# Optimization experiments

Measured on AMD Instinct MI355X. Metric: run time of the kernel, lower is better.

Reference implementation:

```python
import jax, jax.numpy as jnp
import numpy as np

N_QUBITS = 12
N_LAYERS = 3
N_CHUNKS = 12
CHUNK = 4
BATCH = 2048


def _u3(theta, phi, lam):
    # PennyLane U3 = [[cos(t/2), -e^{i l} sin(t/2)], [e^{i p} sin(t/2), e^{i(p+l)} cos(t/2)]]
    ct = jnp.cos(theta / 2).astype(jnp.complex64)
    st = jnp.sin(theta / 2).astype(jnp.complex64)
    ep = jnp.exp(1j * phi.astype(jnp.complex64))
    el = jnp.exp(1j * lam.astype(jnp.complex64))
    return jnp.stack([jnp.stack([ct, -el * st]), jnp.stack([ep * st, ep * el * ct])])


def _apply_1q(state, U, w):
    # state: (2,)*N_QUBITS
    s = jnp.moveaxis(state, w, 0)
    s = jnp.tensordot(U, s, axes=1)
    return jnp.moveaxis(s, 0, w)


def _apply_cnot(state, c, t):
    s = jnp.moveaxis(state, (c, t), (0, 1))
    s = jnp.stack([s[0], jnp.flip(s[1], axis=0)], axis=0)
    return jnp.moveaxis(s, (0, 1), (c, t))


def _circuit(params):
    # params: [N_CHUNKS, 3] -> expval PauliZ per wire, shape [N_QUBITS]
    state = jnp.zeros((2,) * N_QUBITS, jnp.complex64).at[(0,) * N_QUBITS].set(1.0)
    for _ in range(N_LAYERS):
        for i in range(N_CHUNKS):
            state = _apply_1q(state, _u3(params[i, 0], params[i, 1], params[i, 2]), i)
        for i in range(N_QUBITS):
            state = _apply_cnot(state, i, (i + 1) % N_QUBITS)
    p = jnp.abs(state) ** 2
    sign = jnp.array([1.0, -1.0], p.dtype)
    zs = []
    for i in range(N_QUBITS):
        marg = p.sum(axis=tuple(a for a in range(N_QUBITS) if a != i))
        zs.append(jnp.dot(marg, sign))
    return jnp.stack(zs)


def setup_inputs() -> dict:
    key = jax.random.key(0)
    ks = jax.random.split(key, 7)
    return {
        "x": jax.random.normal(ks[0], (BATCH, 48), jnp.float32),
        "reupload_weights": jax.random.normal(ks[1], (N_CHUNKS, 3, CHUNK), jnp.float32) * 0.1,
        "reupload_bias": jax.random.normal(ks[2], (N_CHUNKS, 3), jnp.float32) * 0.1,
        "w1": jax.random.normal(ks[3], (64, N_QUBITS), jnp.float32) * 0.1,
        "b1": jax.random.normal(ks[4], (64,), jnp.float32) * 0.1,
        "w2": jax.random.normal(ks[5], (256, 64), jnp.float32) * 0.1,
        "b2": jax.random.normal(ks[6], (256,), jnp.float32) * 0.1,
    }


def reference(x, reupload_weights, reupload_bias, w1, b1, w2, b2):
    chunks = x.reshape(-1, N_CHUNKS, CHUNK)  # [B, 12, 4]
    # per-chunk affine map: [12,3,4] @ [B,12,4] -> [B,12,3]
    params = jnp.einsum("cpk,bck->bcp", reupload_weights, chunks) + reupload_bias
    qz = jax.vmap(_circuit)(params)  # [B, 12]
    h = jax.nn.relu(qz @ w1.T + b1)
    return h @ w2.T + b2
```

## Files before the change

kernel.cpp:

```cpp
#include <hip/hip_runtime.h>
#include <hip/hip_fp16.h>
#include <math.h>

typedef _Float16 half8 __attribute__((ext_vector_type(8)));
typedef float f32x4 __attribute__((ext_vector_type(4)));

__device__ __forceinline__ int finv12(int c) {
    return ((c ^ (c << 1)) & 0xFFF) ^ ((c >> 11) * 3);
}
__device__ __forceinline__ int sg0(int s) { return s ^ (((s >> 8) & 1) << 4) ^ (((s >> 9) & 1) << 6); }
__device__ __forceinline__ int sg1(int s) { return s ^ (((s >> 12) & 3) << 4) ^ (((s >> 7) & 1) << 6); }
__device__ __forceinline__ int sg2(int s) { return s ^ (((s >> 8) & 7) << 4); }

__global__ __attribute__((amdgpu_flat_work_group_size(256, 256)))
void qparam_kernel(const float* __restrict__ x, const float* __restrict__ rw,
                   const float* __restrict__ rb, float* __restrict__ uo, int total)
{
    const int g = blockIdx.x * 256 + threadIdx.x;
    if (g >= total) return;
    const int c = g % 12;
    const float4 xv = ((const float4*)x)[g];
    float prm[3];
    #pragma unroll
    for (int p = 0; p < 3; ++p) {
        const float4 wv = ((const float4*)rw)[c * 3 + p];
        prm[p] = rb[c * 3 + p] + wv.x * xv.x + wv.y * xv.y + wv.z * xv.z + wv.w * xv.w;
    }
    float st_, ct_; sincosf(0.5f * prm[0], &st_, &ct_);
    float sp_, cp_; sincosf(prm[1], &sp_, &cp_);
    float sl_, cl_; sincosf(prm[2], &sl_, &cl_);
    const float cpl = cp_ * cl_ - sp_ * sl_;
    const float spl = sp_ * cl_ + cp_ * sl_;
    ((float4*)uo)[g * 2]     = make_float4(ct_, 0.0f, -cl_ * st_, -sl_ * st_);
    ((float4*)uo)[g * 2 + 1] = make_float4(cp_ * st_, sp_ * st_, cpl * ct_, spl * ct_);
}

template<int G>
__device__ __forceinline__ void mfma_pass(
    const char* __restrict__ ldb, char* __restrict__ stb,
    half8 arh, half8 arl, half8 aih, half8 ail,
    int t, int l15, int q, int wv, bool first, bool last,
    float& A0, float& AT0, float& AT01, float& AR0, float& AR01)
{
    #pragma unroll
    for (int T = 0; T < 4; ++T) {
        const int tt = wv * 4 + T;
        half8 bfr;
        if (first) {
            half8 z = {};
            if (t == 0 && T == 0) z[0] = (_Float16)1.0f;
            bfr = z;
        } else {
            int raw4[4];
            #pragma unroll
            for (int j = 0; j < 4; ++j) {
                int byte_;
                if (G == 0) {
                    const int ap = finv12(j | (q << 2) | (l15 << 4) | (tt << 8));
                    byte_ = sg2(64 * (ap & 255) + 4 * ((ap >> 8) & 15));
                } else if (G == 1) {
                    byte_ = sg0(256 * q + 64 * j + 1024 * tt + 4 * l15);
                } else {
                    byte_ = sg1(64 * l15 + 4096 * q + 1024 * j + 4 * tt);
                }
                raw4[j] = *(const int*)(ldb + byte_);
            }
            __builtin_memcpy(&bfr, raw4, 16);
        }
        f32x4 cre = {0.f, 0.f, 0.f, 0.f}, cim = {0.f, 0.f, 0.f, 0.f};
        cre = __builtin_amdgcn_mfma_f32_16x16x32_f16(arh, bfr, cre, 0, 0, 0);
        cre = __builtin_amdgcn_mfma_f32_16x16x32_f16(arl, bfr, cre, 0, 0, 0);
        cim = __builtin_amdgcn_mfma_f32_16x16x32_f16(aih, bfr, cim, 0, 0, 0);
        cim = __builtin_amdgcn_mfma_f32_16x16x32_f16(ail, bfr, cim, 0, 0, 0);
        if (!last) {
            unsigned int ov4[4];
            #pragma unroll
            for (int r = 0; r < 4; ++r) {
                __half2 hp = __floats2half2_rn(cre[r], cim[r]);
                ov4[r] = *(unsigned int*)&hp;
            }
            int4 ov;
            __builtin_memcpy(&ov, ov4, 16);
            const int sb = 1024 * tt + 64 * l15 + 16 * q;
            const int sbyte = (G == 0) ? sg0(sb) : (G == 1) ? sg1(sb) : sg2(sb);
            *(int4*)(stb + sbyte) = ov;
        } else {
            const int sT0 = T & 1, sT01 = (T ^ (T >> 1)) & 1;
            #pragma unroll
            for (int r = 0; r < 4; ++r) {
                const float pr = cre[r] * cre[r] + cim[r] * cim[r];
                A0 += pr;
                AT0  += sT0 ? -pr : pr;
                AT01 += sT01 ? -pr : pr;
                AR0  += (sT01 ^ (r & 1)) ? -pr : pr;
                AR01 += (sT01 ^ ((r ^ (r >> 1)) & 1)) ? -pr : pr;
            }
        }
    }
}

__global__ __attribute__((amdgpu_flat_work_group_size(256, 256), amdgpu_waves_per_eu(4, 4)))
void qreup_kernel(const float* __restrict__ uin,
                  const float* __restrict__ w1, const float* __restrict__ b1,
                  const float* __restrict__ w2, const float* __restrict__ b2,
                  float* __restrict__ out)
{
    __shared__ __align__(16) char lds[38912];
    char* const buf0 = lds;
    char* const buf1 = lds + 16384;
    char* const wl   = lds + 32768;

    const int t = threadIdx.x;
    const int b = blockIdx.x;
    const float* __restrict__ ub = uin + b * 96;
    const int l15 = t & 15, q = (t >> 4) & 3, wv = t >> 6;

    {
        const int mp = t >> 4, mm = t & 15;
        #pragma unroll
        for (int g = 0; g < 3; ++g) {
            const float* p0 = ub + g * 32 + ((mp & 1) * 4 + (mm & 1) * 2);
            float wr = p0[0], wi = p0[1];
            #pragma unroll
            for (int bq = 1; bq < 4; ++bq) {
                const float* p = ub + g * 32 + bq * 8 + ((mp >> bq) & 1) * 4 + ((mm >> bq) & 1) * 2;
                const float br = p[0], bi = p[1];
                const float nr = wr * br - wi * bi, ni = wr * bi + wi * br;
                wr = nr; wi = ni;
            }
            const _Float16 hr = (_Float16)wr, hi_ = (_Float16)wi;
            const _Float16 lr = (_Float16)(wr - (float)hr), li = (_Float16)(wi - (float)hi_);
            union { _Float16 h[2]; unsigned int u; } ph, pl_;
            ph.h[0] = hr;  ph.h[1] = hi_;
            pl_.h[0] = lr; pl_.h[1] = li;
            *(unsigned int*)(wl + g * 2048 +        mp * 64 + mm * 4) = ph.u;
            *(unsigned int*)(wl + g * 2048 + 1024 + mp * 64 + mm * 4) = pl_.u;
        }
    }
    __syncthreads();

    half8 ArH[3], ArL[3], AiH[3], AiL[3];
    #pragma unroll
    for (int g = 0; g < 3; ++g) {
        #pragma unroll
        for (int hl = 0; hl < 2; ++hl) {
            int4 raw = *(const int4*)(wl + g * 2048 + hl * 1024 + l15 * 64 + q * 16);
            int re4[4], im4[4];
            int rr[4] = {raw.x, raw.y, raw.z, raw.w};
            #pragma unroll
            for (int i = 0; i < 4; ++i) {
                re4[i] = rr[i] ^ 0x80000000;
                im4[i] = (int)(((unsigned)rr[i] >> 16) | ((unsigned)rr[i] << 16));
            }
            half8 hre, him;
            __builtin_memcpy(&hre, re4, 16);
            __builtin_memcpy(&him, im4, 16);
            if (hl == 0) { ArH[g] = hre; AiH[g] = him; }
            else         { ArL[g] = hre; AiL[g] = him; }
        }
    }

    float A0 = 0.f, AT0 = 0.f, AT01 = 0.f, AR0 = 0.f, AR01 = 0.f;
    #pragma unroll 1
    for (int L = 0; L < 3; ++L) {
        char* const bA = (L & 1) ? buf1 : buf0;
        char* const bB = (L & 1) ? buf0 : buf1;
        if (L) __syncthreads();
        mfma_pass<0>(bB, bA, ArH[0], ArL[0], AiH[0], AiL[0], t, l15, q, wv,
                     L == 0, false, A0, AT0, AT01, AR0, AR01);
        __syncthreads();
        mfma_pass<1>(bA, bB, ArH[1], ArL[1], AiH[1], AiL[1], t, l15, q, wv,
                     false, false, A0, AT0, AT01, AR0, AR01);
        __syncthreads();
        mfma_pass<2>(bB, bA, ArH[2], ArL[2], AiH[2], AiL[2], t, l15, q, wv,
                     false, L == 2, A0, AT0, AT01, AR0, AR01);
    }

    const int pl = __popc(l15) & 1;
    const int wv0 = wv & 1, wv1 = (wv >> 1) & 1, wv01 = wv0 ^ wv1;
    const int q0 = q & 1, q1 = (q >> 1) & 1;
    float zp[12];
    zp[1] = (__popc(l15 & 3) & 1) ? -A0 : A0;
    zp[2] = (__popc(l15 & 7) & 1) ? -A0 : A0;
    zp[3] = pl ? -A0 : A0;
    zp[4] = pl ? -AT0 : AT0;
    zp[5] = pl ? -AT01 : AT01;
    zp[6] = (pl ^ wv0) ? -AT01 : AT01;
    zp[7] = (pl ^ wv0 ^ wv1) ? -AT01 : AT01;
    zp[8] = (pl ^ wv01) ? -AR0 : AR0;
    zp[9] = (pl ^ wv01) ? -AR01 : AR01;
    zp[10] = (pl ^ wv01 ^ q0) ? -AR01 : AR01;
    zp[11] = (pl ^ wv01 ^ q0 ^ q1) ? -AR01 : AR01;
    zp[0]  = ((l15 & 1) ^ pl ^ wv01 ^ q0 ^ q1) ? -AR01 : AR01;

    #pragma unroll
    for (int i = 0; i < 12; ++i) {
        float vv = zp[i];
        #pragma unroll
        for (int off = 32; off > 0; off >>= 1)
            vv += __shfl_xor(vv, off, 64);
        zp[i] = vv;
    }

    __syncthreads();
    float* stf  = (float*)lds;
    float* zred = stf;
    float* qzs  = stf + 48;
    float* hbuf = stf + 64;

    if ((t & 63) == 0) {
        #pragma unroll
        for (int i = 0; i < 12; ++i) zred[wv * 12 + i] = zp[i];
    }
    __syncthreads();
    if (t < 12)
        qzs[t] = zred[t] + zred[12 + t] + zred[24 + t] + zred[36 + t];
    __syncthreads();

    if (t < 64) {
        float acc = b1[t];
        #pragma unroll
        for (int i = 0; i < 12; ++i) acc += qzs[i] * w1[t * 12 + i];
        hbuf[t] = fmaxf(acc, 0.0f);
    }
    __syncthreads();
    float acc = b2[t];
    #pragma unroll 4
    for (int k4 = 0; k4 < 16; ++k4) {
        const float4 wvv = ((const float4*)w2)[t * 16 + k4];
        acc += wvv.x * hbuf[k4 * 4 + 0] + wvv.y * hbuf[k4 * 4 + 1]
             + wvv.z * hbuf[k4 * 4 + 2] + wvv.w * hbuf[k4 * 4 + 3];
    }
    out[b * 256 + t] = acc;
}

extern "C" void kernel_launch(void* const* d_in, const int* in_sizes, int n_in,
                              void* d_out, int out_size, void* d_ws, size_t ws_size,
                              hipStream_t stream) {
    const float* x  = (const float*)d_in[0];
    const float* rw = (const float*)d_in[1];
    const float* rb = (const float*)d_in[2];
    const float* w1 = (const float*)d_in[3];
    const float* b1 = (const float*)d_in[4];
    const float* w2 = (const float*)d_in[5];
    const float* b2 = (const float*)d_in[6];
    float* out = (float*)d_out;
    float* uws = (float*)d_ws;

    const int batch = in_sizes[0] / 48;
    const int total = batch * 12;
    qparam_kernel<<<(total + 255) / 256, 256, 0, stream>>>(x, rw, rb, uws, total);
    qreup_kernel<<<batch, 256, 0, stream>>>(uws, w1, b1, w2, b2, out);
}
```

Baseline: 111.7 us.

## Redesign LDS state layout so MFMA B-fragments load as single 16-byte reads

Changes the shared-memory layout of the statevector between the three MFMA gate-group passes. Each B-operand fragment is now read with one int4 load, using an XOR swizzle plus a conditional word swap, instead of four scattered 4-byte reads with permuted addresses. Writes become four 4-byte scattered stores per tile instead of one 16-byte store, and the CNOT permutation is folded into the final pass's store addressing. The aim is fewer LDS read instructions and less address arithmetic, at the cost of more store instructions, possible bank conflicts, and added index complexity.

```diff
diff --git a/kernel.cpp b/kernel.cpp
--- a/kernel.cpp
+++ b/kernel.cpp
@@ -5,12 +5,9 @@
 typedef _Float16 half8 __attribute__((ext_vector_type(8)));
 typedef float f32x4 __attribute__((ext_vector_type(4)));
 
-__device__ __forceinline__ int finv12(int c) {
-    return ((c ^ (c << 1)) & 0xFFF) ^ ((c >> 11) * 3);
-}
-__device__ __forceinline__ int sg0(int s) { return s ^ (((s >> 8) & 1) << 4) ^ (((s >> 9) & 1) << 6); }
-__device__ __forceinline__ int sg1(int s) { return s ^ (((s >> 12) & 3) << 4) ^ (((s >> 7) & 1) << 6); }
-__device__ __forceinline__ int sg2(int s) { return s ^ (((s >> 8) & 7) << 4); }
+__device__ __forceinline__ int pfx4(int x) {
+    return (x ^ (x << 1) ^ (x << 2) ^ (x << 3)) & 15;
+}
 
 __global__ __attribute__((amdgpu_flat_work_group_size(256, 256)))
 void qparam_kernel(const float* __restrict__ x, const float* __restrict__ rw,
@@ -35,80 +32,14 @@
     ((float4*)uo)[g * 2 + 1] = make_float4(cp_ * st_, sp_ * st_, cpl * ct_, spl * ct_);
 }
 
-template<int G>
-__device__ __forceinline__ void mfma_pass(
-    const char* __restrict__ ldb, char* __restrict__ stb,
-    half8 arh, half8 arl, half8 aih, half8 ail,
-    int t, int l15, int q, int wv, bool first, bool last,
-    float& A0, float& AT0, float& AT01, float& AR0, float& AR01)
-{
-    #pragma unroll
-    for (int T = 0; T < 4; ++T) {
-        const int tt = wv * 4 + T;
-        half8 bfr;
-        if (first) {
-            half8 z = {};
-            if (t == 0 && T == 0) z[0] = (_Float16)1.0f;
-            bfr = z;
-        } else {
-            int raw4[4];
-            #pragma unroll
-            for (int j = 0; j < 4; ++j) {
-                int byte_;
-                if (G == 0) {
-                    const int ap = finv12(j | (q << 2) | (l15 << 4) | (tt << 8));
-                    byte_ = sg2(64 * (ap & 255) + 4 * ((ap >> 8) & 15));
-                } else if (G == 1) {
-                    byte_ = sg0(256 * q + 64 * j + 1024 * tt + 4 * l15);
-                } else {
-                    byte_ = sg1(64 * l15 + 4096 * q + 1024 * j + 4 * tt);
-                }
-                raw4[j] = *(const int*)(ldb + byte_);
-            }
-            __builtin_memcpy(&bfr, raw4, 16);
-        }
-        f32x4 cre = {0.f, 0.f, 0.f, 0.f}, cim = {0.f, 0.f, 0.f, 0.f};
-        cre = __builtin_amdgcn_mfma_f32_16x16x32_f16(arh, bfr, cre, 0, 0, 0);
-        cre = __builtin_amdgcn_mfma_f32_16x16x32_f16(arl, bfr, cre, 0, 0, 0);
-        cim = __builtin_amdgcn_mfma_f32_16x16x32_f16(aih, bfr, cim, 0, 0, 0);
-        cim = __builtin_amdgcn_mfma_f32_16x16x32_f16(ail, bfr, cim, 0, 0, 0);
-        if (!last) {
-            unsigned int ov4[4];
-            #pragma unroll
-            for (int r = 0; r < 4; ++r) {
-                __half2 hp = __floats2half2_rn(cre[r], cim[r]);
-                ov4[r] = *(unsigned int*)&hp;
-            }
-            int4 ov;
-            __builtin_memcpy(&ov, ov4, 16);
-            const int sb = 1024 * tt + 64 * l15 + 16 * q;
-            const int sbyte = (G == 0) ? sg0(sb) : (G == 1) ? sg1(sb) : sg2(sb);
-            *(int4*)(stb + sbyte) = ov;
-        } else {
-            const int sT0 = T & 1, sT01 = (T ^ (T >> 1)) & 1;
-            #pragma unroll
-            for (int r = 0; r < 4; ++r) {
-                const float pr = cre[r] * cre[r] + cim[r] * cim[r];
-                A0 += pr;
-                AT0  += sT0 ? -pr : pr;
-                AT01 += sT01 ? -pr : pr;
-                AR0  += (sT01 ^ (r & 1)) ? -pr : pr;
-                AR01 += (sT01 ^ ((r ^ (r >> 1)) & 1)) ? -pr : pr;
-            }
-        }
-    }
-}
-
 __global__ __attribute__((amdgpu_flat_work_group_size(256, 256), amdgpu_waves_per_eu(4, 4)))
 void qreup_kernel(const float* __restrict__ uin,
                   const float* __restrict__ w1, const float* __restrict__ b1,
                   const float* __restrict__ w2, const float* __restrict__ b2,
                   float* __restrict__ out)
 {
-    __shared__ __align__(16) char lds[38912];
-    char* const buf0 = lds;
-    char* const buf1 = lds + 16384;
-    char* const wl   = lds + 32768;
+    __shared__ __align__(16) char lds[32768];
+    char* const wl = lds;
 
     const int t = threadIdx.x;
     const int b = blockIdx.x;
@@ -160,20 +91,120 @@
         }
     }
 
+    const int Ml = pfx4(l15);
+    const int piL = (Ml >> 3) & 1;
+
     float A0 = 0.f, AT0 = 0.f, AT01 = 0.f, AR0 = 0.f, AR01 = 0.f;
+    char* rbuf = lds;
+    char* wbuf = lds + 16384;
+
     #pragma unroll 1
     for (int L = 0; L < 3; ++L) {
-        char* const bA = (L & 1) ? buf1 : buf0;
-        char* const bB = (L & 1) ? buf0 : buf1;
         if (L) __syncthreads();
-        mfma_pass<0>(bB, bA, ArH[0], ArL[0], AiH[0], AiL[0], t, l15, q, wv,
-                     L == 0, false, A0, AT0, AT01, AR0, AR01);
+        #pragma unroll
+        for (int T = 0; T < 4; ++T) {
+            const int tt = wv * 4 + T;
+            half8 bfr;
+            if (L == 0) {
+                half8 z = {};
+                if (t == 0 && T == 0) z[0] = (_Float16)1.0f;
+                bfr = z;
+            } else {
+                const int nu = 16 * tt + l15;
+                const int al = ((l15 >> 1) & 1) | ((((l15 >> 1) ^ (l15 >> 2)) & 1) << 1);
+                const int be = ((tt >> 1) ^ (tt >> 2)) & 1;
+                int4 raw = *(const int4*)(rbuf + 64 * (nu ^ be) + 16 * (q ^ al));
+                if (tt & 8) {
+                    int tmp = raw.x; raw.x = raw.y; raw.y = tmp;
+                    tmp = raw.z; raw.z = raw.w; raw.w = tmp;
+                }
+                __builtin_memcpy(&bfr, &raw, 16);
+            }
+            f32x4 cre = {0.f,0.f,0.f,0.f}, cim = {0.f,0.f,0.f,0.f};
+            cre = __builtin_amdgcn_mfma_f32_16x16x32_f16(ArH[0], bfr, cre, 0, 0, 0);
+            cre = __builtin_amdgcn_mfma_f32_16x16x32_f16(ArL[0], bfr, cre, 0, 0, 0);
+            cim = __builtin_amdgcn_mfma_f32_16x16x32_f16(AiH[0], bfr, cim, 0, 0, 0);
+            cim = __builtin_amdgcn_mfma_f32_16x16x32_f16(AiL[0], bfr, cim, 0, 0, 0);
+            const int als = q ^ ((tt >> 1) & 3);
+            const int bes = (tt ^ q) & 1;
+            const int D = 4 * (l15 ^ (als << 2));
+            #pragma unroll
+            for (int r = 0; r < 4; ++r) {
+                const int nu = (4 * q + r) + 16 * tt;
+                __half2 hp = __floats2half2_rn(cre[r], cim[r]);
+                *(unsigned int*)(wbuf + 64 * (nu ^ bes) + D) = *(unsigned int*)&hp;
+            }
+        }
+        { char* tmp = rbuf; rbuf = wbuf; wbuf = tmp; }
+
         __syncthreads();
-        mfma_pass<1>(bA, bB, ArH[1], ArL[1], AiH[1], AiL[1], t, l15, q, wv,
-                     false, false, A0, AT0, AT01, AR0, AR01);
+        #pragma unroll
+        for (int T = 0; T < 4; ++T) {
+            const int tt = wv * 4 + T;
+            const int nu = tt + 16 * l15;
+            const int al = ((tt >> 2) & 3) ^ ((l15 >> 1) & 3);
+            const int be = (l15 ^ (tt >> 2)) & 1;
+            int4 raw = *(const int4*)(rbuf + 64 * (nu ^ be) + 16 * (q ^ al));
+            half8 bfr; __builtin_memcpy(&bfr, &raw, 16);
+            f32x4 cre = {0.f,0.f,0.f,0.f}, cim = {0.f,0.f,0.f,0.f};
+            cre = __builtin_amdgcn_mfma_f32_16x16x32_f16(ArH[1], bfr, cre, 0, 0, 0);
+            cre = __builtin_amdgcn_mfma_f32_16x16x32_f16(ArL[1], bfr, cre, 0, 0, 0);
+            cim = __builtin_amdgcn_mfma_f32_16x16x32_f16(AiH[1], bfr, cim, 0, 0, 0);
+            cim = __builtin_amdgcn_mfma_f32_16x16x32_f16(AiL[1], bfr, cim, 0, 0, 0);
+            const int als = ((tt >> 1) & 3) ^ q;
+            const int bes = q & 1;
+            const int D = 4 * (l15 ^ (als << 2));
+            #pragma unroll
+            for (int r = 0; r < 4; ++r) {
+                const int nu2 = tt + 16 * (4 * q + r);
+                __half2 hp = __floats2half2_rn(cre[r], cim[r]);
+                *(unsigned int*)(wbuf + 64 * (nu2 ^ bes) + D) = *(unsigned int*)&hp;
+            }
+        }
+        { char* tmp = rbuf; rbuf = wbuf; wbuf = tmp; }
+
         __syncthreads();
-        mfma_pass<2>(bB, bA, ArH[2], ArL[2], AiH[2], AiL[2], t, l15, q, wv,
-                     false, L == 2, A0, AT0, AT01, AR0, AR01);
+        #pragma unroll
+        for (int T = 0; T < 4; ++T) {
+            const int tt = wv * 4 + T;
+            const int nu = l15 + 16 * tt;
+            const int al = ((l15 >> 1) & 3) ^ ((tt >> 2) & 3);
+            const int be = (tt >> 2) & 1;
+            int4 raw = *(const int4*)(rbuf + 64 * (nu ^ be) + 16 * (q ^ al));
+            half8 bfr; __builtin_memcpy(&bfr, &raw, 16);
+            f32x4 cre = {0.f,0.f,0.f,0.f}, cim = {0.f,0.f,0.f,0.f};
+            cre = __builtin_amdgcn_mfma_f32_16x16x32_f16(ArH[2], bfr, cre, 0, 0, 0);
+            cre = __builtin_amdgcn_mfma_f32_16x16x32_f16(ArL[2], bfr, cre, 0, 0, 0);
+            cim = __builtin_amdgcn_mfma_f32_16x16x32_f16(AiH[2], bfr, cim, 0, 0, 0);
+            cim = __builtin_amdgcn_mfma_f32_16x16x32_f16(AiL[2], bfr, cim, 0, 0, 0);
+            if (L < 2) {
+                const int taub = pfx4(tt);
+                const int lowH = (piL ? 15 : 0) ^ taub;
+                const int s    = (lowH >> 3) & 1;
+                const int als  = ((lowH >> 1) & 1) | ((((lowH >> 1) ^ (lowH >> 2)) & 1) << 1);
+                const int bes  = q & 1;
+                const int D = 4 * (Ml ^ (als << 2));
+                #pragma unroll
+                for (int r = 0; r < 4; ++r) {
+                    const int rho = pfx4(4 * q + r);
+                    const int H = lowH | (((s ? 15 : 0) ^ rho) << 4);
+                    __half2 hp = __floats2half2_rn(cre[r], cim[r]);
+                    *(unsigned int*)(wbuf + 64 * (H ^ bes) + D) = *(unsigned int*)&hp;
+                }
+            } else {
+                const int sT0 = T & 1, sT01 = (T ^ (T >> 1)) & 1;
+                #pragma unroll
+                for (int r = 0; r < 4; ++r) {
+                    const float pr = cre[r] * cre[r] + cim[r] * cim[r];
+                    A0 += pr;
+                    AT0  += sT0 ? -pr : pr;
+                    AT01 += sT01 ? -pr : pr;
+                    AR0  += (sT01 ^ (r & 1)) ? -pr : pr;
+                    AR01 += (sT01 ^ ((r ^ (r >> 1)) & 1)) ? -pr : pr;
+                }
+            }
+        }
+        { char* tmp = rbuf; rbuf = wbuf; wbuf = tmp; }
     }
 
     const int pl = __popc(l15) & 1;
```

Result: faster. 100.2 us (-10.3%).
